# Performance work log

Measured on AMD Instinct MI355X. Metric: run time of the kernel, lower is better.

## Reference

```python
import jax, jax.numpy as jnp
import numpy as np
import math

B, S, IN_DIM, OUT_DIM = 16, 1024, 512, 256
THETA = 10000.0


def _rope_single(x, cos, sin):
    # x: [B,S,D]; cos/sin: [D//2] -- SAME rotation applied at every position
    # (faithful to original: freqs_cis[seq_len*2] selects a single row)
    xr = x.reshape(x.shape[0], x.shape[1], -1, 2)
    a, b = xr[..., 0], xr[..., 1]
    out = jnp.stack([a * cos - b * sin, a * sin + b * cos], axis=-1)
    return out.reshape(x.shape)


def setup_inputs() -> dict:
    key = jax.random.key(0)
    ks = jax.random.split(key, 4)
    scale = 1.0 / math.sqrt(IN_DIM)
    x = jax.random.normal(ks[0], (B, S, IN_DIM), jnp.float32)
    wq = jax.random.normal(ks[1], (OUT_DIM, IN_DIM), jnp.float32) * scale
    wk = jax.random.normal(ks[2], (OUT_DIM, IN_DIM), jnp.float32) * scale
    wv = jax.random.normal(ks[3], (OUT_DIM, IN_DIM), jnp.float32) * scale
    bq = jnp.zeros((OUT_DIM,), jnp.float32)
    bk = jnp.zeros((OUT_DIM,), jnp.float32)
    bv = jnp.zeros((OUT_DIM,), jnp.float32)
    return {"x": x, "wq": wq, "bq": bq, "wk": wk, "bk": bk, "wv": wv, "bv": bv}


def reference(x, wq, bq, wk, bk, wv, bv):
    dim = x.shape[-1]  # scale uses INPUT dim, per original code
    # freqs_cis row at position index = 2*seq_len
    inv_freq = 1.0 / (THETA ** (jnp.arange(0, OUT_DIM, 2, dtype=jnp.float32) / OUT_DIM))
    angle = (2.0 * S) * inv_freq  # [OUT_DIM//2]
    cos, sin = jnp.cos(angle), jnp.sin(angle)

    q = jnp.einsum('bsi,oi->bso', x, wq) + bq
    k = jnp.einsum('bsi,oi->bso', x, wk) + bk
    v = jnp.einsum('bsi,oi->bso', x, wv) + bv

    q = _rope_single(q, cos, sin)
    k = _rope_single(k, cos, sin)

    scores = jnp.einsum('bqd,bkd->bqk', q, k) / jnp.sqrt(jnp.float32(dim))
    scores = jax.nn.softmax(scores.astype(jnp.float32), axis=-1)
    out = jnp.einsum('bqk,bkd->bqd', scores, v)
    return out
```

## Files before the change

kernel.cpp:

```cpp
#include <hip/hip_runtime.h>
#include <hip/hip_bf16.h>


typedef __attribute__((ext_vector_type(8))) short short8;
typedef __attribute__((ext_vector_type(4))) short short4v;
typedef __attribute__((ext_vector_type(4))) float f32x4;

#define GLL16(g, l)                                                            \
  __builtin_amdgcn_global_load_lds(                                            \
      (const __attribute__((address_space(1))) unsigned int*)(g),              \
      (__attribute__((address_space(3))) unsigned int*)(l), 16, 0, 0)

static __device__ __forceinline__ short f2bf(float f) {
  __hip_bfloat16 h = __float2bfloat16(f);
  return __builtin_bit_cast(short, h);
}

__global__ void cvt_x(const float* __restrict__ src, short* __restrict__ dst, int n8) {
  int i = blockIdx.x * blockDim.x + threadIdx.x;
  int stride = gridDim.x * blockDim.x;
  for (; i < n8; i += stride) {
    const float4* sp = reinterpret_cast<const float4*>(src) + i * 2;
    float4 a = sp[0], b = sp[1];
    short8 o;
    o[0] = f2bf(a.x); o[1] = f2bf(a.y); o[2] = f2bf(a.z); o[3] = f2bf(a.w);
    o[4] = f2bf(b.x); o[5] = f2bf(b.y); o[6] = f2bf(b.z); o[7] = f2bf(b.w);
    *(reinterpret_cast<short8*>(dst) + i) = o;
  }
}

__global__ void cvt_w(const float* __restrict__ wq, const float* __restrict__ wk,
                      const float* __restrict__ wv, short* __restrict__ dst) {
  int i = blockIdx.x * blockDim.x + threadIdx.x;
  if (i >= 49152) return;
  const float* src;
  int off;
  if (i < 16384)      { src = wq; off = i; }
  else if (i < 32768) { src = wk; off = i - 16384; }
  else                { src = wv; off = i - 32768; }
  const float4* sp = reinterpret_cast<const float4*>(src) + off * 2;
  float4 a = sp[0], b = sp[1];
  short8 o;
  o[0] = f2bf(a.x); o[1] = f2bf(a.y); o[2] = f2bf(a.z); o[3] = f2bf(a.w);
  o[4] = f2bf(b.x); o[5] = f2bf(b.y); o[6] = f2bf(b.z); o[7] = f2bf(b.w);
  *(reinterpret_cast<short8*>(dst) + i) = o;
}

__global__ __launch_bounds__(256) void qkv_gemm(
    const short* __restrict__ xb, const short* __restrict__ wb,
    const float* __restrict__ bq, const float* __restrict__ bk,
    const float* __restrict__ bv, short* __restrict__ qb,
    short* __restrict__ kb, short* __restrict__ vt) {
  __shared__ __align__(16) char smem[32768];
  const int bid = blockIdx.x;
  const int swz = (bid & 7) * 96 + (bid >> 3);
  const int mt = swz / 6, nt = swz % 6;
  const int tid = threadIdx.x;
  const int w = tid >> 6, lane = tid & 63;
  const int g = lane >> 4, c = lane & 15;
  const int wm = w >> 1, wn = w & 1;

  f32x4 acc[4][4];
  const f32x4 fzero = {0.f, 0.f, 0.f, 0.f};
#pragma unroll
  for (int mi = 0; mi < 4; mi++)
#pragma unroll
    for (int ni = 0; ni < 4; ni++) acc[mi][ni] = fzero;

  for (int kk = 0; kk < 8; ++kk) {
    __syncthreads();
#pragma unroll
    for (int i = 0; i < 8; i++) {
      int idx = w * 8 + i;
      int r = (idx & 15) * 8 + (lane >> 3);
      int cc = lane & 7;
      const short* src;
      if (idx < 16)
        src = xb + (mt * 128 + r) * 512 + kk * 64 + ((cc ^ (r & 7)) * 8);
      else
        src = wb + (nt * 128 + r) * 512 + kk * 64 + ((cc ^ (r & 7)) * 8);
      GLL16(src, smem + idx * 1024);
    }
    asm volatile("s_waitcnt vmcnt(0)" ::: "memory");
    __syncthreads();
#pragma unroll
    for (int ks = 0; ks < 2; ++ks) {
      short8 af[4], bf[4];
#pragma unroll
      for (int mi = 0; mi < 4; mi++) {
        int row = wm * 64 + mi * 16 + c;
        af[mi] = *(const short8*)(smem + row * 128 + (((ks * 4 + g) ^ (row & 7)) * 16));
      }
#pragma unroll
      for (int ni = 0; ni < 4; ni++) {
        int row = wn * 64 + ni * 16 + c;
        bf[ni] = *(const short8*)(smem + 16384 + row * 128 + (((ks * 4 + g) ^ (row & 7)) * 16));
      }
#pragma unroll
      for (int mi = 0; mi < 4; mi++)
#pragma unroll
        for (int ni = 0; ni < 4; ni++)
          acc[mi][ni] = __builtin_amdgcn_mfma_f32_16x16x32_bf16(af[mi], bf[ni], acc[mi][ni], 0, 0, 0);
    }
  }

  const int colbase = nt * 128 + wn * 64;
  const int cls = colbase >> 8;
  const int cw = colbase & 255;
  const int rowbase = mt * 128 + wm * 64;
  if (cls == 0) {
#pragma unroll
    for (int mi = 0; mi < 4; mi++)
#pragma unroll
      for (int ni = 0; ni < 4; ni++) {
        int col = cw + ni * 16 + c;
        float bias = bq[col];
#pragma unroll
        for (int j = 0; j < 4; j++) {
          int row = rowbase + mi * 16 + g * 4 + j;
          qb[row * 256 + col] = f2bf((acc[mi][ni][j] + bias) * 0.044194173824159216f);
        }
      }
  } else if (cls == 1) {
#pragma unroll
    for (int mi = 0; mi < 4; mi++)
#pragma unroll
      for (int ni = 0; ni < 4; ni++) {
        int col = cw + ni * 16 + c;
        float bias = bk[col];
#pragma unroll
        for (int j = 0; j < 4; j++) {
          int row = rowbase + mi * 16 + g * 4 + j;
          kb[row * 256 + col] = f2bf(acc[mi][ni][j] + bias);
        }
      }
  } else {
#pragma unroll
    for (int mi = 0; mi < 4; mi++)
#pragma unroll
      for (int ni = 0; ni < 4; ni++) {
        int d = cw + ni * 16 + c;
        float bias = bv[d];
        int r0 = rowbase + mi * 16 + g * 4;
        int bb = r0 >> 10, s0 = r0 & 1023;
        short4v o;
        o[0] = f2bf(acc[mi][ni][0] + bias);
        o[1] = f2bf(acc[mi][ni][1] + bias);
        o[2] = f2bf(acc[mi][ni][2] + bias);
        o[3] = f2bf(acc[mi][ni][3] + bias);
        *(short4v*)(vt + (bb * 256 + d) * 1024 + s0) = o;
      }
  }
}

__global__ __launch_bounds__(256) void attn_kernel(
    const short* __restrict__ qb, const short* __restrict__ kb,
    const short* __restrict__ vt, float* __restrict__ out) {
  __shared__ __align__(16) char smem[74752];
  const int bid = blockIdx.x;
  const int swz = (bid & 7) * 32 + (bid >> 3);
  const int b = swz >> 4, qt = swz & 15;
  const int tid = threadIdx.x;
  const int w = tid >> 6, lane = tid & 63;
  const int g = lane >> 4, c = lane & 15;
  const int q0 = b * 1024 + qt * 64 + w * 16;
  const int VB = 32768, PB = 65536;
  short* sp = (short*)(smem + PB + w * 2304);

  short8 qf[8];
#pragma unroll
  for (int ks = 0; ks < 8; ks++)
    qf[ks] = *(const short8*)(qb + (q0 + c) * 256 + ks * 32 + g * 8);

  f32x4 O[16];
  const f32x4 fzero = {0.f, 0.f, 0.f, 0.f};
#pragma unroll
  for (int ni = 0; ni < 16; ni++) O[ni] = fzero;
  float m_[4] = {-1e30f, -1e30f, -1e30f, -1e30f};
  float l_[4] = {0.f, 0.f, 0.f, 0.f};

  for (int kt = 0; kt < 16; ++kt) {
    __syncthreads();
    if (w < 2) {
#pragma unroll
      for (int i = 0; i < 16; i++) {
        int j = w * 16 + i;
        int r = j * 2 + (lane >> 5);
        int cc = lane & 31;
        const short* src = kb + (b * 1024 + kt * 64 + r) * 256 + ((cc ^ (r & 7)) * 8);
        GLL16(src, smem + j * 1024);
      }
    } else {
#pragma unroll
      for (int i = 0; i < 16; i++) {
        int j = (w - 2) * 16 + i;
        int r = j * 8 + (lane >> 3);
        int cc = lane & 7;
        const short* src = vt + (b * 256 + r) * 1024 + kt * 64 + ((cc ^ (r & 7)) * 8);
        GLL16(src, smem + VB + j * 1024);
      }
    }
    asm volatile("s_waitcnt vmcnt(0)" ::: "memory");
    __syncthreads();

    f32x4 Sf[4];
#pragma unroll
    for (int nf = 0; nf < 4; nf++) Sf[nf] = fzero;
#pragma unroll
    for (int ks = 0; ks < 8; ks++) {
      short8 kf[4];
#pragma unroll
      for (int nf = 0; nf < 4; nf++) {
        int key = nf * 16 + c;
        kf[nf] = *(const short8*)(smem + key * 512 + (((ks * 4 + g) ^ (c & 7)) * 16));
      }
#pragma unroll
      for (int nf = 0; nf < 4; nf++)
        Sf[nf] = __builtin_amdgcn_mfma_f32_16x16x32_bf16(qf[ks], kf[nf], Sf[nf], 0, 0, 0);
    }

    float Pv[4][4], scl[4];
#pragma unroll
    for (int j = 0; j < 4; j++) {
      float tm = fmaxf(fmaxf(Sf[0][j], Sf[1][j]), fmaxf(Sf[2][j], Sf[3][j]));
      tm = fmaxf(tm, __shfl_xor(tm, 1));
      tm = fmaxf(tm, __shfl_xor(tm, 2));
      tm = fmaxf(tm, __shfl_xor(tm, 4));
      tm = fmaxf(tm, __shfl_xor(tm, 8));
      float nm = fmaxf(m_[j], tm);
      scl[j] = __expf(m_[j] - nm);
      m_[j] = nm;
      float rs = 0.f;
#pragma unroll
      for (int nf = 0; nf < 4; nf++) {
        float p = __expf(Sf[nf][j] - nm);
        Pv[nf][j] = p;
        rs += p;
      }
      rs += __shfl_xor(rs, 1);
      rs += __shfl_xor(rs, 2);
      rs += __shfl_xor(rs, 4);
      rs += __shfl_xor(rs, 8);
      l_[j] = l_[j] * scl[j] + rs;
    }
#pragma unroll
    for (int ni = 0; ni < 16; ni++) {
      O[ni][0] *= scl[0]; O[ni][1] *= scl[1];
      O[ni][2] *= scl[2]; O[ni][3] *= scl[3];
    }

#pragma unroll
    for (int nf = 0; nf < 4; nf++)
#pragma unroll
      for (int j = 0; j < 4; j++)
        sp[(g * 4 + j) * 72 + nf * 16 + c] = f2bf(Pv[nf][j]);

    short8 pf[2];
#pragma unroll
    for (int ks2 = 0; ks2 < 2; ks2++)
      pf[ks2] = *(const short8*)((char*)sp + c * 144 + ks2 * 64 + g * 16);

#pragma unroll
    for (int ni = 0; ni < 16; ni++) {
      int d = ni * 16 + c;
#pragma unroll
      for (int ks2 = 0; ks2 < 2; ks2++) {
        short8 vf = *(const short8*)(smem + VB + d * 128 + (((ks2 * 4 + g) ^ (c & 7)) * 16));
        O[ni] = __builtin_amdgcn_mfma_f32_16x16x32_bf16(pf[ks2], vf, O[ni], 0, 0, 0);
      }
    }
  }

#pragma unroll
  for (int j = 0; j < 4; j++) {
    float inv = 1.0f / l_[j];
    int row = q0 + g * 4 + j;
#pragma unroll
    for (int ni = 0; ni < 16; ni++)
      out[row * 256 + ni * 16 + c] = O[ni][j] * inv;
  }
}

extern "C" void kernel_launch(void* const* d_in, const int* in_sizes, int n_in,
                              void* d_out, int out_size, void* d_ws, size_t ws_size,
                              hipStream_t stream) {
  const float* x  = (const float*)d_in[0];
  const float* wq = (const float*)d_in[1];
  const float* bq = (const float*)d_in[2];
  const float* wk = (const float*)d_in[3];
  const float* bk = (const float*)d_in[4];
  const float* wv = (const float*)d_in[5];
  const float* bv = (const float*)d_in[6];
  float* out = (float*)d_out;
  char* ws = (char*)d_ws;
  short* xb = (short*)ws;
  short* wb = (short*)(ws + 16777216);
  short* qb = (short*)(ws + 17563648);
  short* kb = (short*)(ws + 25952256);
  short* vt = (short*)(ws + 34340864);

  cvt_x<<<2048, 256, 0, stream>>>(x, xb, 1048576);
  cvt_w<<<192, 256, 0, stream>>>(wq, wk, wv, wb);
  qkv_gemm<<<768, 256, 0, stream>>>(xb, wb, bq, bk, bv, qb, kb, vt);
  attn_kernel<<<256, 256, 0, stream>>>(qb, kb, vt, out);
}
```

Measured before the change: 168.6 us.

## Fuse x bf16 conversion into QKV GEMM, transpose V via LDS, double-buffer attention

Removes the separate x-to-bf16 conversion kernel and converts fp32 x in registers while staging the GEMM A tile into LDS. The V epilogue now transposes through LDS so the transposed V is written with 16-byte coalesced stores. The attention kernel double-buffers K/V tiles in LDS, prefetching the next tile during compute. The trade-offs are more fp32 reads of x (re-read per N tile), synchronous global loads in the GEMM, and doubled attention LDS use, which limits occupancy.

```diff
diff --git a/kernel.cpp b/kernel.cpp
--- a/kernel.cpp
+++ b/kernel.cpp
@@ -14,19 +14,6 @@
 static __device__ __forceinline__ short f2bf(float f) {
   __hip_bfloat16 h = __float2bfloat16(f);
   return __builtin_bit_cast(short, h);
-}
-
-__global__ void cvt_x(const float* __restrict__ src, short* __restrict__ dst, int n8) {
-  int i = blockIdx.x * blockDim.x + threadIdx.x;
-  int stride = gridDim.x * blockDim.x;
-  for (; i < n8; i += stride) {
-    const float4* sp = reinterpret_cast<const float4*>(src) + i * 2;
-    float4 a = sp[0], b = sp[1];
-    short8 o;
-    o[0] = f2bf(a.x); o[1] = f2bf(a.y); o[2] = f2bf(a.z); o[3] = f2bf(a.w);
-    o[4] = f2bf(b.x); o[5] = f2bf(b.y); o[6] = f2bf(b.z); o[7] = f2bf(b.w);
-    *(reinterpret_cast<short8*>(dst) + i) = o;
-  }
 }
 
 __global__ void cvt_w(const float* __restrict__ wq, const float* __restrict__ wk,
@@ -47,7 +34,7 @@
 }
 
 __global__ __launch_bounds__(256) void qkv_gemm(
-    const short* __restrict__ xb, const short* __restrict__ wb,
+    const float* __restrict__ x, const short* __restrict__ wb,
     const float* __restrict__ bq, const float* __restrict__ bk,
     const float* __restrict__ bv, short* __restrict__ qb,
     short* __restrict__ kb, short* __restrict__ vt) {
@@ -67,19 +54,33 @@
 #pragma unroll
     for (int ni = 0; ni < 4; ni++) acc[mi][ni] = fzero;
 
+  const int arow = tid >> 4;
+  const int acol4 = tid & 15;
+  const int achunk = acol4 >> 1, ahalf = (tid & 1) * 8;
+
   for (int kk = 0; kk < 8; ++kk) {
     __syncthreads();
 #pragma unroll
-    for (int i = 0; i < 8; i++) {
-      int idx = w * 8 + i;
-      int r = (idx & 15) * 8 + (lane >> 3);
+    for (int i = 0; i < 4; i++) {
+      int idx = w * 4 + i;
+      int r = idx * 8 + (lane >> 3);
       int cc = lane & 7;
-      const short* src;
-      if (idx < 16)
-        src = xb + (mt * 128 + r) * 512 + kk * 64 + ((cc ^ (r & 7)) * 8);
-      else
-        src = wb + (nt * 128 + r) * 512 + kk * 64 + ((cc ^ (r & 7)) * 8);
-      GLL16(src, smem + idx * 1024);
+      GLL16(wb + (nt * 128 + r) * 512 + kk * 64 + ((cc ^ (r & 7)) * 8),
+            smem + 16384 + idx * 1024);
+    }
+    float4 xv[8];
+#pragma unroll
+    for (int j = 0; j < 8; j++) {
+      int row = j * 16 + arow;
+      xv[j] = *(const float4*)(x + (mt * 128 + row) * 512 + kk * 64 + acol4 * 4);
+    }
+#pragma unroll
+    for (int j = 0; j < 8; j++) {
+      int row = j * 16 + arow;
+      short4v s4;
+      s4[0] = f2bf(xv[j].x); s4[1] = f2bf(xv[j].y);
+      s4[2] = f2bf(xv[j].z); s4[3] = f2bf(xv[j].w);
+      *(short4v*)(smem + row * 128 + ((achunk ^ (row & 7)) * 16) + ahalf) = s4;
     }
     asm volatile("s_waitcnt vmcnt(0)" ::: "memory");
     __syncthreads();
@@ -110,53 +111,61 @@
   const int rowbase = mt * 128 + wm * 64;
   if (cls == 0) {
 #pragma unroll
-    for (int mi = 0; mi < 4; mi++)
-#pragma unroll
-      for (int ni = 0; ni < 4; ni++) {
-        int col = cw + ni * 16 + c;
-        float bias = bq[col];
+    for (int ni = 0; ni < 4; ni++) {
+      int col = cw + ni * 16 + c;
+      float bias = bq[col];
+#pragma unroll
+      for (int mi = 0; mi < 4; mi++)
 #pragma unroll
         for (int j = 0; j < 4; j++) {
           int row = rowbase + mi * 16 + g * 4 + j;
           qb[row * 256 + col] = f2bf((acc[mi][ni][j] + bias) * 0.044194173824159216f);
         }
-      }
+    }
   } else if (cls == 1) {
 #pragma unroll
-    for (int mi = 0; mi < 4; mi++)
-#pragma unroll
-      for (int ni = 0; ni < 4; ni++) {
-        int col = cw + ni * 16 + c;
-        float bias = bk[col];
+    for (int ni = 0; ni < 4; ni++) {
+      int col = cw + ni * 16 + c;
+      float bias = bk[col];
+#pragma unroll
+      for (int mi = 0; mi < 4; mi++)
 #pragma unroll
         for (int j = 0; j < 4; j++) {
           int row = rowbase + mi * 16 + g * 4 + j;
           kb[row * 256 + col] = f2bf(acc[mi][ni][j] + bias);
         }
-      }
+    }
   } else {
-#pragma unroll
-    for (int mi = 0; mi < 4; mi++)
-#pragma unroll
-      for (int ni = 0; ni < 4; ni++) {
-        int d = cw + ni * 16 + c;
-        float bias = bv[d];
-        int r0 = rowbase + mi * 16 + g * 4;
-        int bb = r0 >> 10, s0 = r0 & 1023;
-        short4v o;
-        o[0] = f2bf(acc[mi][ni][0] + bias);
-        o[1] = f2bf(acc[mi][ni][1] + bias);
-        o[2] = f2bf(acc[mi][ni][2] + bias);
-        o[3] = f2bf(acc[mi][ni][3] + bias);
-        *(short4v*)(vt + (bb * 256 + d) * 1024 + s0) = o;
-      }
+    __syncthreads();
+    char* tb = smem + w * 8192;
+#pragma unroll
+    for (int ni = 0; ni < 4; ni++) {
+      int dl = ni * 16 + c;
+      float bias = bv[cw + dl];
+#pragma unroll
+      for (int mi = 0; mi < 4; mi++)
+#pragma unroll
+        for (int j = 0; j < 4; j++) {
+          int sl = mi * 16 + g * 4 + j;
+          *(short*)(tb + dl * 128 + ((sl * 2) ^ ((dl & 7) << 4))) =
+              f2bf(acc[mi][ni][j] + bias);
+        }
+    }
+    const int bb = rowbase >> 10, sb = rowbase & 1023;
+#pragma unroll
+    for (int i = 0; i < 8; i++) {
+      int dl = i * 8 + (lane >> 3);
+      int ch = lane & 7;
+      short8 val = *(const short8*)(tb + dl * 128 + (((ch ^ (dl & 7)) * 16)));
+      *(short8*)(vt + (bb * 256 + cw + dl) * 1024 + sb + ch * 8) = val;
+    }
   }
 }
 
 __global__ __launch_bounds__(256) void attn_kernel(
     const short* __restrict__ qb, const short* __restrict__ kb,
     const short* __restrict__ vt, float* __restrict__ out) {
-  __shared__ __align__(16) char smem[74752];
+  __shared__ __align__(16) char smem[140288];
   const int bid = blockIdx.x;
   const int swz = (bid & 7) * 32 + (bid >> 3);
   const int b = swz >> 4, qt = swz & 15;
@@ -164,7 +173,7 @@
   const int w = tid >> 6, lane = tid & 63;
   const int g = lane >> 4, c = lane & 15;
   const int q0 = b * 1024 + qt * 64 + w * 16;
-  const int VB = 32768, PB = 65536;
+  const int VB = 65536, PB = 131072;
   short* sp = (short*)(smem + PB + w * 2304);
 
   short8 qf[8];
@@ -179,16 +188,15 @@
   float m_[4] = {-1e30f, -1e30f, -1e30f, -1e30f};
   float l_[4] = {0.f, 0.f, 0.f, 0.f};
 
-  for (int kt = 0; kt < 16; ++kt) {
-    __syncthreads();
+  auto stage = [&](int kt, int bsel) {
     if (w < 2) {
 #pragma unroll
       for (int i = 0; i < 16; i++) {
         int j = w * 16 + i;
         int r = j * 2 + (lane >> 5);
         int cc = lane & 31;
-        const short* src = kb + (b * 1024 + kt * 64 + r) * 256 + ((cc ^ (r & 7)) * 8);
-        GLL16(src, smem + j * 1024);
+        GLL16(kb + (b * 1024 + kt * 64 + r) * 256 + ((cc ^ (r & 7)) * 8),
+              smem + bsel * 32768 + j * 1024);
       }
     } else {
 #pragma unroll
@@ -196,12 +204,20 @@
         int j = (w - 2) * 16 + i;
         int r = j * 8 + (lane >> 3);
         int cc = lane & 7;
-        const short* src = vt + (b * 256 + r) * 1024 + kt * 64 + ((cc ^ (r & 7)) * 8);
-        GLL16(src, smem + VB + j * 1024);
-      }
-    }
+        GLL16(vt + (b * 256 + r) * 1024 + kt * 64 + ((cc ^ (r & 7)) * 8),
+              smem + VB + bsel * 32768 + j * 1024);
+      }
+    }
+  };
+
+  stage(0, 0);
+  for (int kt = 0; kt < 16; ++kt) {
+    const int cur = kt & 1;
+    const char* kbase = smem + cur * 32768;
+    const char* vbase = smem + VB + cur * 32768;
     asm volatile("s_waitcnt vmcnt(0)" ::: "memory");
     __syncthreads();
+    if (kt < 15) stage(kt + 1, cur ^ 1);
 
     f32x4 Sf[4];
 #pragma unroll
@@ -212,7 +228,7 @@
 #pragma unroll
       for (int nf = 0; nf < 4; nf++) {
         int key = nf * 16 + c;
-        kf[nf] = *(const short8*)(smem + key * 512 + (((ks * 4 + g) ^ (c & 7)) * 16));
+        kf[nf] = *(const short8*)(kbase + key * 512 + (((ks * 4 + g) ^ (c & 7)) * 16));
       }
 #pragma unroll
       for (int nf = 0; nf < 4; nf++)
@@ -265,7 +281,7 @@
       int d = ni * 16 + c;
 #pragma unroll
       for (int ks2 = 0; ks2 < 2; ks2++) {
-        short8 vf = *(const short8*)(smem + VB + d * 128 + (((ks2 * 4 + g) ^ (c & 7)) * 16));
+        short8 vf = *(const short8*)(vbase + d * 128 + (((ks2 * 4 + g) ^ (c & 7)) * 16));
         O[ni] = __builtin_amdgcn_mfma_f32_16x16x32_bf16(pf[ks2], vf, O[ni], 0, 0, 0);
       }
     }
@@ -293,14 +309,12 @@
   const float* bv = (const float*)d_in[6];
   float* out = (float*)d_out;
   char* ws = (char*)d_ws;
-  short* xb = (short*)ws;
-  short* wb = (short*)(ws + 16777216);
-  short* qb = (short*)(ws + 17563648);
-  short* kb = (short*)(ws + 25952256);
-  short* vt = (short*)(ws + 34340864);
-
-  cvt_x<<<2048, 256, 0, stream>>>(x, xb, 1048576);
+  short* wb = (short*)ws;
+  short* qb = (short*)(ws + 786432);
+  short* kb = (short*)(ws + 9175040);
+  short* vt = (short*)(ws + 17563648);
+
   cvt_w<<<192, 256, 0, stream>>>(wq, wk, wv, wb);
-  qkv_gemm<<<768, 256, 0, stream>>>(xb, wb, bq, bk, bv, qb, kb, vt);
+  qkv_gemm<<<768, 256, 0, stream>>>(x, wb, bq, bk, bv, qb, kb, vt);
   attn_kernel<<<256, 256, 0, stream>>>(qb, kb, vt, out);
 }
```

Result: no change. 167.0 us (-0.9%).
